# Kernel tuning notes

Hardware: AMD Instinct MI355X
Metric: run time of the kernel (lower is better)

The kernel has to match this reference:

```python
import jax, jax.numpy as jnp
import numpy as np

WEIGHT_THRESH = 0.5
EPS = 1e-5


def setup_inputs() -> dict:
    key = jax.random.key(0)
    k1, k2, k3 = jax.random.split(key, 3)
    B, N = 4096, 2048
    src_points = jax.random.normal(k1, (B, N, 3), dtype=jnp.float32)
    tgt_points = jax.random.normal(k2, (B, N, 3), dtype=jnp.float32)
    weights = jax.random.uniform(k3, (B, N), dtype=jnp.float32)
    return {"src_points": src_points, "tgt_points": tgt_points, "weights": weights}


def reference(src_points, tgt_points, weights):
    # threshold + normalize weights: (B, N)
    w = jnp.where(weights < WEIGHT_THRESH, jnp.zeros_like(weights), weights)
    w = w / (jnp.sum(w, axis=1, keepdims=True) + EPS)
    w = w[:, :, None]  # (B, N, 1)

    # weighted centroids (B, 1, 3)
    src_centroid = jnp.sum(src_points * w, axis=1, keepdims=True)
    ref_centroid = jnp.sum(tgt_points * w, axis=1, keepdims=True)
    src_c = src_points - src_centroid
    ref_c = tgt_points - ref_centroid

    # cross-covariance H = src_c^T @ (w * ref_c): (B, 3, 3)
    H = jnp.einsum("bnd,bne->bde", src_c, w * ref_c)

    U, _, Vh = jnp.linalg.svd(H)
    V = jnp.swapaxes(Vh, -1, -2)
    Ut = jnp.swapaxes(U, -1, -2)

    # sign correction: R = V @ diag(1,1,sign(det(V Ut))) @ Ut
    s = jnp.sign(jnp.linalg.det(V @ Ut))  # (B,)
    d = jnp.stack([jnp.ones_like(s), jnp.ones_like(s), s], axis=-1)  # (B, 3)
    R = (V * d[:, None, :]) @ Ut  # scale columns of V

    t = ref_centroid[:, 0, :] - jnp.einsum("bij,bj->bi", R, src_centroid[:, 0, :])
    return R, t
```

## Files before the change

kernel.cpp:

```cpp
#include <hip/hip_runtime.h>
#include <math.h>

#define NPTS 2048
#define THREADS 256

__global__ __launch_bounds__(THREADS) void wp_reduce_kernel(
    const float* __restrict__ src, const float* __restrict__ tgt,
    const float* __restrict__ w, float* __restrict__ ws)
{
    const int b = blockIdx.x;
    const int tid = threadIdx.x;
    const float* sp = src + (size_t)b * NPTS * 3;
    const float* tp = tgt + (size_t)b * NPTS * 3;
    const float* wp = w + (size_t)b * NPTS;

    float acc[16];
#pragma unroll
    for (int i = 0; i < 16; ++i) acc[i] = 0.f;

#pragma unroll
    for (int it = 0; it < NPTS / (THREADS * 4); ++it) {
        const int n0 = it * (THREADS * 4) + tid * 4;
        const float4 wq = *reinterpret_cast<const float4*>(wp + n0);
        const float4* s4 = reinterpret_cast<const float4*>(sp + 3 * n0);
        const float4 sa = s4[0], sb = s4[1], sc = s4[2];
        const float4* t4 = reinterpret_cast<const float4*>(tp + 3 * n0);
        const float4 ta = t4[0], tb = t4[1], tc = t4[2];

        const float wv[4]   = {wq.x, wq.y, wq.z, wq.w};
        const float sv[12]  = {sa.x, sa.y, sa.z, sa.w, sb.x, sb.y,
                               sb.z, sb.w, sc.x, sc.y, sc.z, sc.w};
        const float tv[12]  = {ta.x, ta.y, ta.z, ta.w, tb.x, tb.y,
                               tb.z, tb.w, tc.x, tc.y, tc.z, tc.w};

#pragma unroll
        for (int k = 0; k < 4; ++k) {
            const float wvk = (wv[k] < 0.5f) ? 0.f : wv[k];
            const float sx = sv[3 * k + 0];
            const float sy = sv[3 * k + 1];
            const float sz = sv[3 * k + 2];
            const float tx = tv[3 * k + 0];
            const float ty = tv[3 * k + 1];
            const float tz = tv[3 * k + 2];
            const float wsx = wvk * sx, wsy = wvk * sy, wsz = wvk * sz;
            acc[0] += wvk;
            acc[1] += wsx; acc[2] += wsy; acc[3] += wsz;
            acc[4] += wvk * tx; acc[5] += wvk * ty; acc[6] += wvk * tz;
            acc[7]  += wsx * tx; acc[8]  += wsx * ty; acc[9]  += wsx * tz;
            acc[10] += wsy * tx; acc[11] += wsy * ty; acc[12] += wsy * tz;
            acc[13] += wsz * tx; acc[14] += wsz * ty; acc[15] += wsz * tz;
        }
    }

#pragma unroll
    for (int off = 32; off >= 1; off >>= 1) {
#pragma unroll
        for (int i = 0; i < 16; ++i)
            acc[i] += __shfl_xor(acc[i], off, 64);
    }

    __shared__ float lds[4][16];
    const int wave = tid >> 6;
    const int lane = tid & 63;
    if (lane == 0) {
#pragma unroll
        for (int i = 0; i < 16; ++i) lds[wave][i] = acc[i];
    }
    __syncthreads();
    if (tid < 16) {
        const float v = lds[0][tid] + lds[1][tid] + lds[2][tid] + lds[3][tid];
        ws[(size_t)b * 16 + tid] = v;
    }
}


template <int P, int Q>
__device__ inline void jrot(double A[3][3], double V[3][3])
{
    const double apq = A[P][Q];
    if (fabs(apq) < 1e-300) return;
    const double theta = (A[Q][Q] - A[P][P]) / (2.0 * apq);
    const double t = ((theta >= 0.0) ? 1.0 : -1.0) /
                     (fabs(theta) + sqrt(theta * theta + 1.0));
    const double c = 1.0 / sqrt(t * t + 1.0);
    const double s = t * c;
#pragma unroll
    for (int k = 0; k < 3; ++k) {
        const double akp = A[k][P], akq = A[k][Q];
        A[k][P] = c * akp - s * akq;
        A[k][Q] = s * akp + c * akq;
    }
#pragma unroll
    for (int k = 0; k < 3; ++k) {
        const double apk = A[P][k], aqk = A[Q][k];
        A[P][k] = c * apk - s * aqk;
        A[Q][k] = s * apk + c * aqk;
    }
#pragma unroll
    for (int k = 0; k < 3; ++k) {
        const double vkp = V[k][P], vkq = V[k][Q];
        V[k][P] = c * vkp - s * vkq;
        V[k][Q] = s * vkp + c * vkq;
    }
}

__device__ inline void matvec3(const double H[3][3], const double v[3], double u[3])
{
#pragma unroll
    for (int i = 0; i < 3; ++i)
        u[i] = H[i][0] * v[0] + H[i][1] * v[1] + H[i][2] * v[2];
}

__device__ inline double dot3(const double a[3], const double b[3])
{
    return a[0] * b[0] + a[1] * b[1] + a[2] * b[2];
}

__device__ inline void cross3(const double a[3], const double b[3], double c[3])
{
    c[0] = a[1] * b[2] - a[2] * b[1];
    c[1] = a[2] * b[0] - a[0] * b[2];
    c[2] = a[0] * b[1] - a[1] * b[0];
}

__global__ void wp_svd_kernel(const float* __restrict__ ws, float* __restrict__ out,
                              int B)
{
    const int b = blockIdx.x * blockDim.x + threadIdx.x;
    if (b >= B) return;

    float s16[16];
#pragma unroll
    for (int i = 0; i < 16; ++i) s16[i] = ws[(size_t)b * 16 + i];

    const double Sw = (double)s16[0];
    const double D = Sw + 1e-5;
    const double invD = 1.0 / D;
    double sc[3], tc[3];
#pragma unroll
    for (int i = 0; i < 3; ++i) {
        sc[i] = (double)s16[1 + i] * invD;
        tc[i] = (double)s16[4 + i] * invD;
    }
    const double f = 2.0 - Sw * invD;

    double H[3][3];
#pragma unroll
    for (int d = 0; d < 3; ++d)
#pragma unroll
        for (int e = 0; e < 3; ++e)
            H[d][e] = (double)s16[7 + 3 * d + e] * invD - sc[d] * tc[e] * f;

    double A[3][3];
#pragma unroll
    for (int i = 0; i < 3; ++i)
#pragma unroll
        for (int j = 0; j < 3; ++j)
            A[i][j] = H[0][i] * H[0][j] + H[1][i] * H[1][j] + H[2][i] * H[2][j];

    double V[3][3] = {{1, 0, 0}, {0, 1, 0}, {0, 0, 1}};
#pragma unroll
    for (int sweep = 0; sweep < 10; ++sweep) {
        jrot<0, 1>(A, V);
        jrot<0, 2>(A, V);
        jrot<1, 2>(A, V);
    }

    const double l0 = A[0][0], l1 = A[1][1], l2 = A[2][2];
    int i0 = 0; double lm = l0;
    if (l1 > lm) { lm = l1; i0 = 1; }
    if (l2 > lm) { lm = l2; i0 = 2; }
    int i2 = 0; double ls = l0;
    if (l1 < ls) { ls = l1; i2 = 1; }
    if (l2 < ls) { ls = l2; i2 = 2; }
    if (i2 == i0) i2 = (i0 + 1) % 3;
    const int i1 = 3 - i0 - i2;

    double v1[3], v2[3], v3[3];
#pragma unroll
    for (int k = 0; k < 3; ++k) {
        v1[k] = V[k][i0];
        v2[k] = V[k][i1];
        v3[k] = V[k][i2];
    }

    double u1[3], u2[3], u3[3];
    matvec3(H, v1, u1);
    const double n1 = sqrt(dot3(u1, u1));
    const double inv1 = 1.0 / fmax(n1, 1e-300);
#pragma unroll
    for (int k = 0; k < 3; ++k) u1[k] *= inv1;

    matvec3(H, v2, u2);
    const double d12 = dot3(u2, u1);
#pragma unroll
    for (int k = 0; k < 3; ++k) u2[k] -= d12 * u1[k];
    double n2 = sqrt(dot3(u2, u2));
    if (n2 < 1e-14 * fmax(n1, 1e-300)) {
        double ax[3] = {1.0, 0.0, 0.0};
        if (fabs(u1[0]) > 0.9) { ax[0] = 0.0; ax[1] = 1.0; }
        cross3(u1, ax, u2);
        n2 = sqrt(dot3(u2, u2));
    }
    const double inv2 = 1.0 / fmax(n2, 1e-300);
#pragma unroll
    for (int k = 0; k < 3; ++k) u2[k] *= inv2;
    cross3(u1, u2, u3);

    double cr[3];
    cross3(v2, v3, cr);
    const double detV = dot3(v1, cr);
    const double s3 = (detV < 0.0) ? -1.0 : 1.0;

    double R[3][3];
#pragma unroll
    for (int i = 0; i < 3; ++i)
#pragma unroll
        for (int j = 0; j < 3; ++j)
            R[i][j] = v1[i] * u1[j] + v2[i] * u2[j] + s3 * v3[i] * u3[j];

    double t[3];
#pragma unroll
    for (int i = 0; i < 3; ++i)
        t[i] = tc[i] - (R[i][0] * sc[0] + R[i][1] * sc[1] + R[i][2] * sc[2]);

    float* outR = out + (size_t)b * 9;
#pragma unroll
    for (int i = 0; i < 3; ++i)
#pragma unroll
        for (int j = 0; j < 3; ++j)
            outR[3 * i + j] = (float)R[i][j];
    float* outT = out + (size_t)B * 9 + (size_t)b * 3;
#pragma unroll
    for (int i = 0; i < 3; ++i) outT[i] = (float)t[i];
}

extern "C" void kernel_launch(void* const* d_in, const int* in_sizes, int n_in,
                              void* d_out, int out_size, void* d_ws, size_t ws_size,
                              hipStream_t stream)
{
    const float* src = (const float*)d_in[0];
    const float* tgt = (const float*)d_in[1];
    const float* w   = (const float*)d_in[2];
    float* out = (float*)d_out;
    float* ws  = (float*)d_ws;
    const int B = in_sizes[2] / NPTS;

    wp_reduce_kernel<<<B, THREADS, 0, stream>>>(src, tgt, w, ws);
    wp_svd_kernel<<<(B + 63) / 64, 64, 0, stream>>>(ws, out, B);
}
```

Measured before the change: 51.69 us.

## Use one wave per batch with double-buffered loads and butterfly reduction

Each batch is now reduced by a single 64-thread wave instead of four waves, so LDS and the block barrier go away. Each lane walks 8 iterations, and the next tile's loads are double-buffered behind the current accumulation. The 16 accumulators are combined with a recursive-halving butterfly (transpose-reduce), which cuts shuffle count. The risk is less parallelism per batch and higher register use per thread, which could lower occupancy or limit how many loads are in flight.

```diff
diff --git a/kernel.cpp b/kernel.cpp
--- a/kernel.cpp
+++ b/kernel.cpp
@@ -2,14 +2,65 @@
 #include <math.h>
 
 #define NPTS 2048
-#define THREADS 256
-
-__global__ __launch_bounds__(THREADS) void wp_reduce_kernel(
+#define T1 64
+#define ITERS (NPTS / (T1 * 4))
+
+
+struct Pts { float4 wq, s0, s1, s2, t0, t1, t2; };
+
+__device__ inline void loadPts(Pts& p, const float* __restrict__ wp,
+                               const float* __restrict__ sp,
+                               const float* __restrict__ tp, int n0)
+{
+    p.wq = *reinterpret_cast<const float4*>(wp + n0);
+    const float4* s4 = reinterpret_cast<const float4*>(sp + 3 * n0);
+    p.s0 = s4[0]; p.s1 = s4[1]; p.s2 = s4[2];
+    const float4* t4 = reinterpret_cast<const float4*>(tp + 3 * n0);
+    p.t0 = t4[0]; p.t1 = t4[1]; p.t2 = t4[2];
+}
+
+__device__ inline void accPts(const Pts& p, float acc[16])
+{
+    const float wv[4]  = {p.wq.x, p.wq.y, p.wq.z, p.wq.w};
+    const float sv[12] = {p.s0.x, p.s0.y, p.s0.z, p.s0.w,
+                          p.s1.x, p.s1.y, p.s1.z, p.s1.w,
+                          p.s2.x, p.s2.y, p.s2.z, p.s2.w};
+    const float tv[12] = {p.t0.x, p.t0.y, p.t0.z, p.t0.w,
+                          p.t1.x, p.t1.y, p.t1.z, p.t1.w,
+                          p.t2.x, p.t2.y, p.t2.z, p.t2.w};
+#pragma unroll
+    for (int k = 0; k < 4; ++k) {
+        const float wvk = (wv[k] < 0.5f) ? 0.f : wv[k];
+        const float sx = sv[3 * k + 0], sy = sv[3 * k + 1], sz = sv[3 * k + 2];
+        const float tx = tv[3 * k + 0], ty = tv[3 * k + 1], tz = tv[3 * k + 2];
+        const float wsx = wvk * sx, wsy = wvk * sy, wsz = wvk * sz;
+        acc[0] += wvk;
+        acc[1] += wsx; acc[2] += wsy; acc[3] += wsz;
+        acc[4] += wvk * tx; acc[5] += wvk * ty; acc[6] += wvk * tz;
+        acc[7]  += wsx * tx; acc[8]  += wsx * ty; acc[9]  += wsx * tz;
+        acc[10] += wsy * tx; acc[11] += wsy * ty; acc[12] += wsy * tz;
+        acc[13] += wsz * tx; acc[14] += wsz * ty; acc[15] += wsz * tz;
+    }
+}
+
+template <int M, int HALF>
+__device__ inline void bflevel(float acc[16], int lane)
+{
+    const bool hi = lane & M;
+#pragma unroll
+    for (int j = 0; j < HALF; ++j) {
+        const float keep = hi ? acc[j + HALF] : acc[j];
+        const float send = hi ? acc[j] : acc[j + HALF];
+        acc[j] = keep + __shfl_xor(send, M, 64);
+    }
+}
+
+__global__ __launch_bounds__(T1, 4) void wp_reduce_kernel(
     const float* __restrict__ src, const float* __restrict__ tgt,
     const float* __restrict__ w, float* __restrict__ ws)
 {
     const int b = blockIdx.x;
-    const int tid = threadIdx.x;
+    const int lane = threadIdx.x;
     const float* sp = src + (size_t)b * NPTS * 3;
     const float* tp = tgt + (size_t)b * NPTS * 3;
     const float* wp = w + (size_t)b * NPTS;
@@ -18,58 +69,31 @@
 #pragma unroll
     for (int i = 0; i < 16; ++i) acc[i] = 0.f;
 
-#pragma unroll
-    for (int it = 0; it < NPTS / (THREADS * 4); ++it) {
-        const int n0 = it * (THREADS * 4) + tid * 4;
-        const float4 wq = *reinterpret_cast<const float4*>(wp + n0);
-        const float4* s4 = reinterpret_cast<const float4*>(sp + 3 * n0);
-        const float4 sa = s4[0], sb = s4[1], sc = s4[2];
-        const float4* t4 = reinterpret_cast<const float4*>(tp + 3 * n0);
-        const float4 ta = t4[0], tb = t4[1], tc = t4[2];
-
-        const float wv[4]   = {wq.x, wq.y, wq.z, wq.w};
-        const float sv[12]  = {sa.x, sa.y, sa.z, sa.w, sb.x, sb.y,
-                               sb.z, sb.w, sc.x, sc.y, sc.z, sc.w};
-        const float tv[12]  = {ta.x, ta.y, ta.z, ta.w, tb.x, tb.y,
-                               tb.z, tb.w, tc.x, tc.y, tc.z, tc.w};
-
-#pragma unroll
-        for (int k = 0; k < 4; ++k) {
-            const float wvk = (wv[k] < 0.5f) ? 0.f : wv[k];
-            const float sx = sv[3 * k + 0];
-            const float sy = sv[3 * k + 1];
-            const float sz = sv[3 * k + 2];
-            const float tx = tv[3 * k + 0];
-            const float ty = tv[3 * k + 1];
-            const float tz = tv[3 * k + 2];
-            const float wsx = wvk * sx, wsy = wvk * sy, wsz = wvk * sz;
-            acc[0] += wvk;
-            acc[1] += wsx; acc[2] += wsy; acc[3] += wsz;
-            acc[4] += wvk * tx; acc[5] += wvk * ty; acc[6] += wvk * tz;
-            acc[7]  += wsx * tx; acc[8]  += wsx * ty; acc[9]  += wsx * tz;
-            acc[10] += wsy * tx; acc[11] += wsy * ty; acc[12] += wsy * tz;
-            acc[13] += wsz * tx; acc[14] += wsz * ty; acc[15] += wsz * tz;
+    Pts A, B;
+    loadPts(A, wp, sp, tp, lane * 4);
+#pragma unroll
+    for (int it = 0; it < ITERS; ++it) {
+        const int n_next = (it + 1) * (T1 * 4) + lane * 4;
+        if (it & 1) {
+            if (it + 1 < ITERS) loadPts(A, wp, sp, tp, n_next);
+            accPts(B, acc);
+        } else {
+            if (it + 1 < ITERS) loadPts(B, wp, sp, tp, n_next);
+            accPts(A, acc);
         }
     }
 
-#pragma unroll
-    for (int off = 32; off >= 1; off >>= 1) {
-#pragma unroll
-        for (int i = 0; i < 16; ++i)
-            acc[i] += __shfl_xor(acc[i], off, 64);
-    }
-
-    __shared__ float lds[4][16];
-    const int wave = tid >> 6;
-    const int lane = tid & 63;
-    if (lane == 0) {
-#pragma unroll
-        for (int i = 0; i < 16; ++i) lds[wave][i] = acc[i];
-    }
-    __syncthreads();
-    if (tid < 16) {
-        const float v = lds[0][tid] + lds[1][tid] + lds[2][tid] + lds[3][tid];
-        ws[(size_t)b * 16 + tid] = v;
+    bflevel<1, 8>(acc, lane);
+    bflevel<2, 4>(acc, lane);
+    bflevel<4, 2>(acc, lane);
+    bflevel<8, 1>(acc, lane);
+    acc[0] += __shfl_xor(acc[0], 16, 64);
+    acc[0] += __shfl_xor(acc[0], 32, 64);
+
+    if (lane < 16) {
+        const int idx = ((lane & 1) << 3) | ((lane & 2) << 1) |
+                        ((lane & 4) >> 1) | ((lane & 8) >> 3);
+        ws[(size_t)b * 16 + idx] = acc[0];
     }
 }
 
@@ -246,6 +270,6 @@
     float* ws  = (float*)d_ws;
     const int B = in_sizes[2] / NPTS;
 
-    wp_reduce_kernel<<<B, THREADS, 0, stream>>>(src, tgt, w, ws);
+    wp_reduce_kernel<<<B, T1, 0, stream>>>(src, tgt, w, ws);
     wp_svd_kernel<<<(B + 63) / 64, 64, 0, stream>>>(ws, out, B);
 }
```

Result: faster. 48.91 us (-5.4%).

## Fuse reduction and SVD kernels, butterfly wave reduction, fewer Jacobi sweeps

Applied to the files above, without the earlier changes.

Merges the per-batch reduction kernel and the 3x3 SVD kernel into one launch, so thread 0 of each block runs the double-precision Jacobi SVD on the block's sums. This removes the second launch and the workspace round-trip. The 16-value wave reduction becomes a butterfly (transpose-style) shuffle pattern that needs fewer shuffles, and the Jacobi sweep count drops from 10 to 8. The trade-off is that the serial FP64 SVD tail now runs inside each reduction block on a single thread, which may keep blocks resident longer.

```diff
diff --git a/kernel.cpp b/kernel.cpp
--- a/kernel.cpp
+++ b/kernel.cpp
@@ -4,9 +4,71 @@
 #define NPTS 2048
 #define THREADS 256
 
-__global__ __launch_bounds__(THREADS) void wp_reduce_kernel(
+
+template <int M, int HALF>
+__device__ inline void bflevel(float acc[16], int lane)
+{
+    const bool hi = lane & M;
+#pragma unroll
+    for (int j = 0; j < HALF; ++j) {
+        const float keep = hi ? acc[j + HALF] : acc[j];
+        const float send = hi ? acc[j] : acc[j + HALF];
+        acc[j] = keep + __shfl_xor(send, M, 64);
+    }
+}
+
+template <int P, int Q>
+__device__ inline void jrot(double A[3][3], double V[3][3])
+{
+    const double apq = A[P][Q];
+    if (fabs(apq) < 1e-300) return;
+    const double theta = (A[Q][Q] - A[P][P]) / (2.0 * apq);
+    const double t = ((theta >= 0.0) ? 1.0 : -1.0) /
+                     (fabs(theta) + sqrt(theta * theta + 1.0));
+    const double c = 1.0 / sqrt(t * t + 1.0);
+    const double s = t * c;
+#pragma unroll
+    for (int k = 0; k < 3; ++k) {
+        const double akp = A[k][P], akq = A[k][Q];
+        A[k][P] = c * akp - s * akq;
+        A[k][Q] = s * akp + c * akq;
+    }
+#pragma unroll
+    for (int k = 0; k < 3; ++k) {
+        const double apk = A[P][k], aqk = A[Q][k];
+        A[P][k] = c * apk - s * aqk;
+        A[Q][k] = s * apk + c * aqk;
+    }
+#pragma unroll
+    for (int k = 0; k < 3; ++k) {
+        const double vkp = V[k][P], vkq = V[k][Q];
+        V[k][P] = c * vkp - s * vkq;
+        V[k][Q] = s * vkp + c * vkq;
+    }
+}
+
+__device__ inline void matvec3(const double H[3][3], const double v[3], double u[3])
+{
+#pragma unroll
+    for (int i = 0; i < 3; ++i)
+        u[i] = H[i][0] * v[0] + H[i][1] * v[1] + H[i][2] * v[2];
+}
+
+__device__ inline double dot3(const double a[3], const double b[3])
+{
+    return a[0] * b[0] + a[1] * b[1] + a[2] * b[2];
+}
+
+__device__ inline void cross3(const double a[3], const double b[3], double c[3])
+{
+    c[0] = a[1] * b[2] - a[2] * b[1];
+    c[1] = a[2] * b[0] - a[0] * b[2];
+    c[2] = a[0] * b[1] - a[1] * b[0];
+}
+
+__global__ __launch_bounds__(THREADS) void wp_fused_kernel(
     const float* __restrict__ src, const float* __restrict__ tgt,
-    const float* __restrict__ w, float* __restrict__ ws)
+    const float* __restrict__ w, float* __restrict__ out, int B)
 {
     const int b = blockIdx.x;
     const int tid = threadIdx.x;
@@ -27,21 +89,17 @@
         const float4* t4 = reinterpret_cast<const float4*>(tp + 3 * n0);
         const float4 ta = t4[0], tb = t4[1], tc = t4[2];
 
-        const float wv[4]   = {wq.x, wq.y, wq.z, wq.w};
-        const float sv[12]  = {sa.x, sa.y, sa.z, sa.w, sb.x, sb.y,
-                               sb.z, sb.w, sc.x, sc.y, sc.z, sc.w};
-        const float tv[12]  = {ta.x, ta.y, ta.z, ta.w, tb.x, tb.y,
-                               tb.z, tb.w, tc.x, tc.y, tc.z, tc.w};
+        const float wv[4]  = {wq.x, wq.y, wq.z, wq.w};
+        const float sv[12] = {sa.x, sa.y, sa.z, sa.w, sb.x, sb.y,
+                              sb.z, sb.w, sc.x, sc.y, sc.z, sc.w};
+        const float tv[12] = {ta.x, ta.y, ta.z, ta.w, tb.x, tb.y,
+                              tb.z, tb.w, tc.x, tc.y, tc.z, tc.w};
 
 #pragma unroll
         for (int k = 0; k < 4; ++k) {
             const float wvk = (wv[k] < 0.5f) ? 0.f : wv[k];
-            const float sx = sv[3 * k + 0];
-            const float sy = sv[3 * k + 1];
-            const float sz = sv[3 * k + 2];
-            const float tx = tv[3 * k + 0];
-            const float ty = tv[3 * k + 1];
-            const float tz = tv[3 * k + 2];
+            const float sx = sv[3 * k + 0], sy = sv[3 * k + 1], sz = sv[3 * k + 2];
+            const float tx = tv[3 * k + 0], ty = tv[3 * k + 1], tz = tv[3 * k + 2];
             const float wsx = wvk * sx, wsy = wvk * sy, wsz = wvk * sz;
             acc[0] += wvk;
             acc[1] += wsx; acc[2] += wsy; acc[3] += wsz;
@@ -52,86 +110,32 @@
         }
     }
 
-#pragma unroll
-    for (int off = 32; off >= 1; off >>= 1) {
-#pragma unroll
-        for (int i = 0; i < 16; ++i)
-            acc[i] += __shfl_xor(acc[i], off, 64);
-    }
-
-    __shared__ float lds[4][16];
     const int wave = tid >> 6;
     const int lane = tid & 63;
-    if (lane == 0) {
-#pragma unroll
-        for (int i = 0; i < 16; ++i) lds[wave][i] = acc[i];
+    bflevel<1, 8>(acc, lane);
+    bflevel<2, 4>(acc, lane);
+    bflevel<4, 2>(acc, lane);
+    bflevel<8, 1>(acc, lane);
+    acc[0] += __shfl_xor(acc[0], 16, 64);
+    acc[0] += __shfl_xor(acc[0], 32, 64);
+
+    __shared__ float lds[4][16];
+    __shared__ float s16f[16];
+    if (lane < 16) {
+        const int idx = ((lane & 1) << 3) | ((lane & 2) << 1) |
+                        ((lane & 4) >> 1) | ((lane & 8) >> 3);
+        lds[wave][idx] = acc[0];
     }
     __syncthreads();
-    if (tid < 16) {
-        const float v = lds[0][tid] + lds[1][tid] + lds[2][tid] + lds[3][tid];
-        ws[(size_t)b * 16 + tid] = v;
-    }
-}
-
-
-template <int P, int Q>
-__device__ inline void jrot(double A[3][3], double V[3][3])
-{
-    const double apq = A[P][Q];
-    if (fabs(apq) < 1e-300) return;
-    const double theta = (A[Q][Q] - A[P][P]) / (2.0 * apq);
-    const double t = ((theta >= 0.0) ? 1.0 : -1.0) /
-                     (fabs(theta) + sqrt(theta * theta + 1.0));
-    const double c = 1.0 / sqrt(t * t + 1.0);
-    const double s = t * c;
-#pragma unroll
-    for (int k = 0; k < 3; ++k) {
-        const double akp = A[k][P], akq = A[k][Q];
-        A[k][P] = c * akp - s * akq;
-        A[k][Q] = s * akp + c * akq;
-    }
-#pragma unroll
-    for (int k = 0; k < 3; ++k) {
-        const double apk = A[P][k], aqk = A[Q][k];
-        A[P][k] = c * apk - s * aqk;
-        A[Q][k] = s * apk + c * aqk;
-    }
-#pragma unroll
-    for (int k = 0; k < 3; ++k) {
-        const double vkp = V[k][P], vkq = V[k][Q];
-        V[k][P] = c * vkp - s * vkq;
-        V[k][Q] = s * vkp + c * vkq;
-    }
-}
-
-__device__ inline void matvec3(const double H[3][3], const double v[3], double u[3])
-{
-#pragma unroll
-    for (int i = 0; i < 3; ++i)
-        u[i] = H[i][0] * v[0] + H[i][1] * v[1] + H[i][2] * v[2];
-}
-
-__device__ inline double dot3(const double a[3], const double b[3])
-{
-    return a[0] * b[0] + a[1] * b[1] + a[2] * b[2];
-}
-
-__device__ inline void cross3(const double a[3], const double b[3], double c[3])
-{
-    c[0] = a[1] * b[2] - a[2] * b[1];
-    c[1] = a[2] * b[0] - a[0] * b[2];
-    c[2] = a[0] * b[1] - a[1] * b[0];
-}
-
-__global__ void wp_svd_kernel(const float* __restrict__ ws, float* __restrict__ out,
-                              int B)
-{
-    const int b = blockIdx.x * blockDim.x + threadIdx.x;
-    if (b >= B) return;
+    if (tid < 16)
+        s16f[tid] = lds[0][tid] + lds[1][tid] + lds[2][tid] + lds[3][tid];
+    __syncthreads();
+
+    if (tid != 0) return;
 
     float s16[16];
 #pragma unroll
-    for (int i = 0; i < 16; ++i) s16[i] = ws[(size_t)b * 16 + i];
+    for (int i = 0; i < 16; ++i) s16[i] = s16f[i];
 
     const double Sw = (double)s16[0];
     const double D = Sw + 1e-5;
@@ -160,7 +164,7 @@
 
     double V[3][3] = {{1, 0, 0}, {0, 1, 0}, {0, 0, 1}};
 #pragma unroll
-    for (int sweep = 0; sweep < 10; ++sweep) {
+    for (int sweep = 0; sweep < 8; ++sweep) {
         jrot<0, 1>(A, V);
         jrot<0, 2>(A, V);
         jrot<1, 2>(A, V);
@@ -243,9 +247,7 @@
     const float* tgt = (const float*)d_in[1];
     const float* w   = (const float*)d_in[2];
     float* out = (float*)d_out;
-    float* ws  = (float*)d_ws;
     const int B = in_sizes[2] / NPTS;
 
-    wp_reduce_kernel<<<B, THREADS, 0, stream>>>(src, tgt, w, ws);
-    wp_svd_kernel<<<(B + 63) / 64, 64, 0, stream>>>(ws, out, B);
-}
+    wp_fused_kernel<<<B, THREADS, 0, stream>>>(src, tgt, w, out, B);
+}
```

Result: slower. 63.97 us (+23.8%).
